# Kernel tuning notes

Measured on AMD Instinct MI355X. Metric: run time of the kernel, lower is better.

The kernel has to match this reference:

```python
import jax, jax.numpy as jnp
import numpy as np

T = 4096
HIDDEN = 2048
N_HEADS = 16
N_KV_HEADS = 4
HEAD_DIM = 128
WINDOW = 1024  # per_layer_sliding_window = WINDOW + 1 -> q attends keys with q_pos - k_pos <= WINDOW
ROPE_THETA = 100000.0
QKV_OUT = (N_HEADS + 2 * N_KV_HEADS) * HEAD_DIM  # 3072


def setup_inputs() -> dict:
    key = jax.random.key(0)
    k1, k2, k3, k4 = jax.random.split(key, 4)
    return {
        "hidden_states": jax.random.normal(k1, (T, HIDDEN), dtype=jnp.float32),
        "positions": jnp.arange(T, dtype=jnp.int32),
        "w_qkv": jax.random.normal(k2, (HIDDEN, QKV_OUT), dtype=jnp.float32) * 0.02,
        "b_qkv": jax.random.normal(k3, (QKV_OUT,), dtype=jnp.float32) * 0.02,
        "w_o": jax.random.normal(k4, (N_HEADS * HEAD_DIM, HIDDEN), dtype=jnp.float32) * 0.02,
    }


def _apply_rope(x, positions):
    # x: [T, n_heads, HEAD_DIM], neox-style rotary over full head dim
    half = HEAD_DIM // 2
    inv_freq = 1.0 / (ROPE_THETA ** (jnp.arange(half, dtype=jnp.float32) / half))
    freqs = positions.astype(jnp.float32)[:, None] * inv_freq[None, :]  # [T, half]
    cos = jnp.cos(freqs)[:, None, :]  # [T, 1, half]
    sin = jnp.sin(freqs)[:, None, :]
    x1, x2 = x[..., :half], x[..., half:]
    return jnp.concatenate([x1 * cos - x2 * sin, x2 * cos + x1 * sin], axis=-1)


def reference(hidden_states, positions, w_qkv, b_qkv, w_o):
    # QKV projection (bias=True)
    qkv = hidden_states @ w_qkv + b_qkv  # [T, QKV_OUT]
    q_size = N_HEADS * HEAD_DIM
    kv_size = N_KV_HEADS * HEAD_DIM
    q = qkv[:, :q_size].reshape(T, N_HEADS, HEAD_DIM)
    k = qkv[:, q_size:q_size + kv_size].reshape(T, N_KV_HEADS, HEAD_DIM)
    v = qkv[:, q_size + kv_size:].reshape(T, N_KV_HEADS, HEAD_DIM)

    # RoPE on q and k
    q = _apply_rope(q, positions)
    k = _apply_rope(k, positions)

    # GQA: expand kv heads to match query heads
    group = N_HEADS // N_KV_HEADS
    k = jnp.repeat(k, group, axis=1)  # [T, N_HEADS, HEAD_DIM]
    v = jnp.repeat(v, group, axis=1)

    scale = HEAD_DIM ** -0.5
    scores = jnp.einsum('qhd,khd->hqk', q, k) * scale  # [H, T, T]

    # causal + sliding-window mask: j <= i and i - j <= WINDOW
    i = jnp.arange(T)[:, None]
    j = jnp.arange(T)[None, :]
    mask = (j <= i) & (i - j <= WINDOW)  # [T, T]
    scores = jnp.where(mask[None, :, :], scores, jnp.finfo(scores.dtype).min)

    probs = jax.nn.softmax(scores, axis=-1)
    attn = jnp.einsum('hqk,khd->qhd', probs, v)  # [T, H, HEAD_DIM]
    attn = attn.reshape(T, N_HEADS * HEAD_DIM)

    # output projection (bias=False)
    return attn @ w_o
```

## Files before the change

kernel.cpp:

```cpp
#include <hip/hip_runtime.h>
#include <cstdint>

#define T_TOK 4096
#define HID 2048
#define NH 16
#define NKV 4
#define HD 128
#define WIN 1024
#define QKVO 3072

typedef float f32x4 __attribute__((ext_vector_type(4)));
typedef __bf16 bf16x8 __attribute__((ext_vector_type(8)));
typedef __bf16 bf16x4 __attribute__((ext_vector_type(4)));
typedef __bf16 bf16x2 __attribute__((ext_vector_type(2)));

__device__ __forceinline__ void gload16(const void* g, void* lds) {
  auto gp = reinterpret_cast<__attribute__((address_space(1))) void*>(
      reinterpret_cast<uintptr_t>(g));
  auto lp = reinterpret_cast<__attribute__((address_space(3))) void*>(
      reinterpret_cast<uintptr_t>(lds));
  __builtin_amdgcn_global_load_lds(gp, lp, 16, 0, 0);
}

__device__ __forceinline__ f32x4 mfma16(bf16x8 a, bf16x8 b, f32x4 c) {
  return __builtin_amdgcn_mfma_f32_16x16x32_bf16(a, b, c, 0, 0, 0);
}

__global__ __launch_bounds__(256) void k_f32_to_bf16(const float* __restrict__ x,
                                                     __bf16* __restrict__ y) {
  const size_t e = (size_t)blockIdx.x * 256 + threadIdx.x;
  const float4* xv = (const float4*)x;
  float4 a = xv[e * 2], b = xv[e * 2 + 1];
  bf16x8 o;
  o[0] = (__bf16)a.x; o[1] = (__bf16)a.y; o[2] = (__bf16)a.z; o[3] = (__bf16)a.w;
  o[4] = (__bf16)b.x; o[5] = (__bf16)b.y; o[6] = (__bf16)b.z; o[7] = (__bf16)b.w;
  *(bf16x8*)(y + e * 8) = o;
}

__global__ __launch_bounds__(256) void k_transpose(const float* __restrict__ W,
                                                   __bf16* __restrict__ Wt,
                                                   int R, int C) {
  __shared__ __bf16 tb[32][33];
  const int nbx = C >> 5;
  const int c0 = (blockIdx.x % nbx) << 5;
  const int r0 = (blockIdx.x / nbx) << 5;
  const int tx = threadIdx.x & 31, ty = threadIdx.x >> 5;
#pragma unroll
  for (int i = 0; i < 32; i += 8)
    tb[ty + i][tx] = (__bf16)W[(size_t)(r0 + ty + i) * C + c0 + tx];
  __syncthreads();
#pragma unroll
  for (int i = 0; i < 32; i += 8)
    Wt[(size_t)(c0 + ty + i) * R + r0 + tx] = tb[tx][ty + i];
}

__global__ void k_rope_tab(const int* __restrict__ pos, float* __restrict__ cosT,
                           float* __restrict__ sinT) {
  const int t = blockIdx.x;
  const int d = threadIdx.x;
  const float inv = exp2f(-(float)d * (16.609640474436812f / 64.0f));
  const float fr = (float)pos[t] * inv;
  cosT[t * 64 + d] = cosf(fr);
  sinT[t * 64 + d] = sinf(fr);
}

template <bool BIAS, typename OutT>
__global__ __launch_bounds__(256, 2) void k_gemm(const __bf16* __restrict__ A,
                                                 const __bf16* __restrict__ Bt,
                                                 const float* __restrict__ bias,
                                                 OutT* __restrict__ C,
                                                 int M, int N, int K) {
  __shared__ __align__(16) __bf16 As[2][128 * 32];
  __shared__ __align__(16) __bf16 Bs[2][128 * 32];
  const int tid = threadIdx.x;
  const int lane = tid & 63;
  const int w = tid >> 6;
  const int wr = w >> 1, wc = w & 1;
  const int c = lane & 15, g = lane >> 4;
  const int gsw = g ^ ((c >> 1) & 3);

  const int nstc = N >> 9;
  const int bid = blockIdx.x;
  const int xcd = bid & 7;
  const int j = bid >> 3;
  const int spx = (int)(gridDim.x >> 7);
  const int s = xcd * spx + (j >> 4);
  const int q = j & 15;
  const int by = (s / nstc) * 4 + (q >> 2);
  const int bx = (s % nstc) * 4 + (q & 3);
  const int m0 = by << 7, n0 = bx << 7;

  const int o0 = w * 2048 + lane * 16;
  const int r0 = o0 >> 6;
  const int g0 = (lane & 3) ^ ((r0 >> 1) & 3);
  const int o1 = o0 + 1024;
  const int r1 = o1 >> 6;
  const int g1 = (lane & 3) ^ ((r1 >> 1) & 3);
  const __bf16* gA0 = A + (size_t)(m0 + r0) * K + g0 * 8;
  const __bf16* gA1 = A + (size_t)(m0 + r1) * K + g1 * 8;
  const __bf16* gB0 = Bt + (size_t)(n0 + r0) * K + g0 * 8;
  const __bf16* gB1 = Bt + (size_t)(n0 + r1) * K + g1 * 8;

  f32x4 acc[4][4] = {};

  {
    char* la = (char*)&As[0][0];
    char* lb = (char*)&Bs[0][0];
    gload16(gA0, la + o0);
    gload16(gA1, la + o1);
    gload16(gB0, lb + o0);
    gload16(gB1, lb + o1);
  }
  __syncthreads();

  int cur = 0;
  for (int kt = 0; kt < K; kt += 32) {
    if (kt + 32 < K) {
      char* la = (char*)&As[0][0] + (cur ^ 1) * 8192;
      char* lb = (char*)&Bs[0][0] + (cur ^ 1) * 8192;
      gload16(gA0 + kt + 32, la + o0);
      gload16(gA1 + kt + 32, la + o1);
      gload16(gB0 + kt + 32, lb + o0);
      gload16(gB1 + kt + 32, lb + o1);
    }
    const __bf16* as = &As[0][0] + cur * 4096;
    const __bf16* bs = &Bs[0][0] + cur * 4096;
    bf16x8 af[4], bfr[4];
#pragma unroll
    for (int mi = 0; mi < 4; mi++)
      af[mi] = *(const bf16x8*)(as + (wr * 64 + mi * 16 + c) * 32 + gsw * 8);
#pragma unroll
    for (int ni = 0; ni < 4; ni++)
      bfr[ni] = *(const bf16x8*)(bs + (wc * 64 + ni * 16 + c) * 32 + gsw * 8);
#pragma unroll
    for (int mi = 0; mi < 4; mi++)
#pragma unroll
      for (int ni = 0; ni < 4; ni++)
        acc[mi][ni] = mfma16(af[mi], bfr[ni], acc[mi][ni]);
    __syncthreads();
    cur ^= 1;
  }

#pragma unroll
  for (int ni = 0; ni < 4; ni++) {
    const int col = n0 + wc * 64 + ni * 16 + c;
    const float bv = BIAS ? bias[col] : 0.0f;
#pragma unroll
    for (int mi = 0; mi < 4; mi++)
#pragma unroll
      for (int r = 0; r < 4; r++) {
        const int row = m0 + wr * 64 + mi * 16 + 4 * g + r;
        C[(size_t)row * N + col] = (OutT)(acc[mi][ni][r] + bv);
      }
  }
}

__global__ __launch_bounds__(256) void k_rope_pack(
    const __bf16* __restrict__ qkv, const float* __restrict__ cosT,
    const float* __restrict__ sinT, __bf16* __restrict__ Qp,
    __bf16* __restrict__ Kp, __bf16* __restrict__ Vt) {
  const int t0 = blockIdx.x * 64;
  const int hh = blockIdx.y;
  const int tid = threadIdx.x;
  const int col0 = hh * HD;
  __shared__ __bf16 lt[64][136];
  if (hh < NH + NKV) {
    const bool isq = hh < NH;
    const float s = isq ? 0.08838834764831845f : 1.0f;
    __bf16* base = isq ? (Qp + (size_t)hh * T_TOK * HD)
                       : (Kp + (size_t)(hh - NH) * T_TOK * HD);
#pragma unroll
    for (int jj = 0; jj < 2; jj++) {
      const int e = jj * 256 + tid;
      const int tl = e >> 3, ch = e & 7;
      const int tt = t0 + tl;
      const bf16x8 x1 = *(const bf16x8*)(qkv + (size_t)tt * QKVO + col0 + ch * 8);
      const bf16x8 x2 = *(const bf16x8*)(qkv + (size_t)tt * QKVO + col0 + 64 + ch * 8);
      const float4 c0 = *(const float4*)(cosT + tt * 64 + ch * 8);
      const float4 c1 = *(const float4*)(cosT + tt * 64 + ch * 8 + 4);
      const float4 s0 = *(const float4*)(sinT + tt * 64 + ch * 8);
      const float4 s1 = *(const float4*)(sinT + tt * 64 + ch * 8 + 4);
      const float cs[8] = {c0.x, c0.y, c0.z, c0.w, c1.x, c1.y, c1.z, c1.w};
      const float sn[8] = {s0.x, s0.y, s0.z, s0.w, s1.x, s1.y, s1.z, s1.w};
      bf16x8 o1, o2;
#pragma unroll
      for (int i = 0; i < 8; i++) {
        const float a = (float)x1[i], b = (float)x2[i];
        o1[i] = (__bf16)((a * cs[i] - b * sn[i]) * s);
        o2[i] = (__bf16)((b * cs[i] + a * sn[i]) * s);
      }
      const int d2s = isq ? ch * 8 : ((ch * 8) ^ ((tt & 7) << 3));
      __bf16* dst = base + (size_t)tt * HD;
      *(bf16x8*)(dst + d2s) = o1;
      *(bf16x8*)(dst + 64 + d2s) = o2;
    }
  } else {
    const int kv = hh - (NH + NKV);
#pragma unroll
    for (int jj = 0; jj < 4; jj++) {
      const int e = jj * 256 + tid;
      const int tl = e >> 4, dc = e & 15;
      *(bf16x8*)&lt[tl][dc * 8] =
          *(const bf16x8*)(qkv + (size_t)(t0 + tl) * QKVO + col0 + dc * 8);
    }
    __syncthreads();
#pragma unroll
    for (int jj = 0; jj < 32; jj++) {
      const int e = jj * 256 + tid;
      const int d = e >> 6, tl = e & 63;
      Vt[((size_t)kv * HD + d) * T_TOK + t0 + (tl ^ ((d & 7) << 3))] = lt[tl][d];
    }
  }
}

__global__ __launch_bounds__(512, 4) void k_attn(const __bf16* __restrict__ Qp,
                                                 const __bf16* __restrict__ Kp,
                                                 const __bf16* __restrict__ Vt,
                                                 __bf16* __restrict__ attnO) {
  __shared__ __align__(16) __bf16 Ks[2][64 * 128];
  __shared__ __align__(16) __bf16 Vs[2][128 * 64];
  __shared__ __align__(16) __bf16 Ps[8][16 * 64];

  const int tid = threadIdx.x;
  const int lane = tid & 63;
  const int w = tid >> 6;
  const int c = lane & 15, g = lane >> 4;
  const int h = blockIdx.y;
  const int kvh = h >> 2;
  const int qb = (int)(gridDim.x - 1) - (int)blockIdx.x;
  const int q0 = qb * 128;
  const int i_row = q0 + w * 16 + c;
  const int swz = (c & 7) << 4;

  bf16x8 qf[4];
  {
    const __bf16* qbase = Qp + ((size_t)h * T_TOK + i_row) * HD;
#pragma unroll
    for (int ds = 0; ds < 4; ds++) qf[ds] = *(const bf16x8*)(qbase + ds * 32 + g * 8);
  }

  f32x4 ot[8] = {};
  float mrun = 0.0f, lrun = 0.0f;

  const int jstart = (q0 >= WIN) ? (q0 - WIN) : 0;
  const int niter = (q0 + 128 - jstart) >> 6;

  const char* Kg = (const char*)Kp + (size_t)kvh * T_TOK * HD * 2;
  const char* Vg = (const char*)Vt + (size_t)kvh * HD * T_TOK * 2;
  const char* kg0 = Kg + (size_t)(jstart + 8 * w + (lane >> 4)) * 256 + (lane & 15) * 16;
  const char* vg0 = Vg + (size_t)(16 * w + (lane >> 3)) * (T_TOK * 2) +
                    (size_t)jstart * 2 + (lane & 7) * 16;

#pragma unroll
  for (int q = 0; q < 2; q++)
    gload16(kg0 + q * 1024, (char*)&Ks[0][0] + w * 2048 + q * 1024);
#pragma unroll
  for (int q = 0; q < 2; q++)
    gload16(vg0 + (size_t)q * 8 * (T_TOK * 2), (char*)&Vs[0][0] + w * 2048 + q * 1024);

  char* pw = (char*)&Ps[w][0];
  int cur = 0;

  for (int it = 0; it < niter; ++it) {
    const int j0 = jstart + it * 64;
    __syncthreads();

    if (it + 1 < niter) {
      const char* kg = kg0 + (size_t)(it + 1) * 16384;
      const char* vg = vg0 + (size_t)(it + 1) * 128;
      char* kd = (char*)&Ks[cur ^ 1][0] + w * 2048;
      char* vd = (char*)&Vs[cur ^ 1][0] + w * 2048;
#pragma unroll
      for (int q = 0; q < 2; q++) gload16(kg + q * 1024, kd + q * 1024);
#pragma unroll
      for (int q = 0; q < 2; q++)
        gload16(vg + (size_t)q * 8 * (T_TOK * 2), vd + q * 1024);
    }

    const char* kb = (const char*)&Ks[cur][0];
    const char* vb = (const char*)&Vs[cur][0];

    f32x4 st[4] = {};
    __builtin_amdgcn_s_setprio(1);
#pragma unroll
    for (int t = 0; t < 4; t++)
#pragma unroll
      for (int ds = 0; ds < 4; ds++) {
        bf16x8 kf = *(const bf16x8*)(kb + (t * 16 + c) * 256 + ((ds * 64 + g * 16) ^ swz));
        st[t] = mfma16(kf, qf[ds], st[t]);
      }
    __builtin_amdgcn_s_setprio(0);

    float p[16];
    float cmax = -1e30f;
    const int jb = i_row - j0 - 4 * g;
#pragma unroll
    for (int t = 0; t < 4; t++)
#pragma unroll
      for (int r = 0; r < 4; r++) {
        float s = st[t][r];
        s = ((unsigned)(jb - 16 * t - r) <= WIN) ? s : -1e30f;
        p[t * 4 + r] = s;
        cmax = fmaxf(cmax, s);
      }
    cmax = fmaxf(cmax, __shfl_xor(cmax, 16));
    cmax = fmaxf(cmax, __shfl_xor(cmax, 32));

    if (!__all(cmax <= mrun + 8.0f)) {
      const float mn = fmaxf(mrun, cmax);
      const float alpha = __expf(mrun - mn);
      lrun *= alpha;
#pragma unroll
      for (int m = 0; m < 8; m++) ot[m] *= alpha;
      mrun = mn;
    }
    float rs = 0.0f;
#pragma unroll
    for (int x = 0; x < 16; x++) {
      const float e_ = __expf(p[x] - mrun);
      p[x] = e_;
      rs += e_;
    }
    rs += __shfl_xor(rs, 16);
    rs += __shfl_xor(rs, 32);
    lrun += rs;

#pragma unroll
    for (int t = 0; t < 4; t++) {
      bf16x4 pk;
      pk[0] = (__bf16)p[t * 4 + 0];
      pk[1] = (__bf16)p[t * 4 + 1];
      pk[2] = (__bf16)p[t * 4 + 2];
      pk[3] = (__bf16)p[t * 4 + 3];
      *(bf16x4*)(pw + c * 128 + ((t * 32 + g * 8) ^ swz)) = pk;
    }
    bf16x8 pf[2];
#pragma unroll
    for (int ks = 0; ks < 2; ks++)
      pf[ks] = *(const bf16x8*)(pw + c * 128 + ((ks * 64 + g * 16) ^ swz));

    __builtin_amdgcn_s_setprio(1);
#pragma unroll
    for (int m = 0; m < 8; m++)
#pragma unroll
      for (int ks = 0; ks < 2; ks++) {
        bf16x8 vf = *(const bf16x8*)(vb + (m * 16 + c) * 128 + ((ks * 64 + g * 16) ^ swz));
        ot[m] = mfma16(vf, pf[ks], ot[m]);
      }
    __builtin_amdgcn_s_setprio(0);

    cur ^= 1;
  }

  const float inv_l = 1.0f / lrun;
  __bf16* orow = attnO + (size_t)i_row * (NH * HD) + h * HD;
#pragma unroll
  for (int m = 0; m < 8; m++) {
    bf16x4 o4;
#pragma unroll
    for (int r = 0; r < 4; r++) o4[r] = (__bf16)(ot[m][r] * inv_l);
    *(bf16x4*)(orow + m * 16 + 4 * g) = o4;
  }
}

extern "C" void kernel_launch(void* const* d_in, const int* in_sizes, int n_in,
                              void* d_out, int out_size, void* d_ws, size_t ws_size,
                              hipStream_t stream) {
  (void)in_sizes; (void)n_in; (void)out_size; (void)ws_size;
  const float* hidden = (const float*)d_in[0];
  const int* positions = (const int*)d_in[1];
  const float* w_qkv = (const float*)d_in[2];
  const float* b_qkv = (const float*)d_in[3];
  const float* w_o = (const float*)d_in[4];
  float* out = (float*)d_out;

  char* ws = (char*)d_ws;
  __bf16* Hb = (__bf16*)ws;    ws += (size_t)T_TOK * HID * 2;
  __bf16* Wqkvt = (__bf16*)ws; ws += (size_t)QKVO * HID * 2;
  __bf16* Wot = (__bf16*)ws;   ws += (size_t)HID * HID * 2;
  float* cosT = (float*)ws;    ws += (size_t)T_TOK * 64 * 4;
  float* sinT = (float*)ws;    ws += (size_t)T_TOK * 64 * 4;
  __bf16* qkv = (__bf16*)ws;   ws += (size_t)T_TOK * QKVO * 2;
  __bf16* Qp = (__bf16*)ws;    ws += (size_t)NH * T_TOK * HD * 2;
  __bf16* Kp = (__bf16*)ws;    ws += (size_t)NKV * T_TOK * HD * 2;
  __bf16* Vt = (__bf16*)ws;    ws += (size_t)NKV * HD * T_TOK * 2;
  __bf16* attnb = (__bf16*)ws; ws += (size_t)T_TOK * NH * HD * 2;

  k_f32_to_bf16<<<T_TOK * HID / (256 * 8), 256, 0, stream>>>(hidden, Hb);
  k_transpose<<<(QKVO / 32) * (HID / 32), 256, 0, stream>>>(w_qkv, Wqkvt, HID, QKVO);
  k_transpose<<<(HID / 32) * (HID / 32), 256, 0, stream>>>(w_o, Wot, HID, HID);
  k_rope_tab<<<T_TOK, 64, 0, stream>>>(positions, cosT, sinT);
  k_gemm<true, __bf16><<<(T_TOK / 128) * (QKVO / 128), 256, 0, stream>>>(
      Hb, Wqkvt, b_qkv, qkv, T_TOK, QKVO, HID);
  k_rope_pack<<<dim3(T_TOK / 64, NH + 2 * NKV), 256, 0, stream>>>(
      qkv, cosT, sinT, Qp, Kp, Vt);
  k_attn<<<dim3(T_TOK / 128, NH), 512, 0, stream>>>(Qp, Kp, Vt, attnb);
  k_gemm<false, float><<<(T_TOK / 128) * (HID / 128), 256, 0, stream>>>(
      attnb, Wot, nullptr, out, T_TOK, HID, HID);
}
```

Baseline: 190.9 us.

## Give each attention wave two query sub-tiles, fold log2e into Q, skip interior masking

The attention kernel drops from 8 waves to 4 waves per block, and each wave now handles 32 query rows as two 16-row sub-tiles. Each K and V fragment read from LDS feeds two MFMAs, which halves LDS fragment traffic per unit of compute. The softmax scale now includes log2(e) so exp2f can replace __expf, and the rescale threshold is adjusted to match. Tiles lying fully inside the causal window skip the per-element mask test. The cost is higher register pressure and fewer waves per block, which may reduce latency hiding.

```diff
diff --git a/kernel.cpp b/kernel.cpp
--- a/kernel.cpp
+++ b/kernel.cpp
@@ -166,7 +166,7 @@
   __shared__ __bf16 lt[64][136];
   if (hh < NH + NKV) {
     const bool isq = hh < NH;
-    const float s = isq ? 0.08838834764831845f : 1.0f;
+    const float s = isq ? (0.08838834764831845f * 1.4426950408889634f) : 1.0f;
     __bf16* base = isq ? (Qp + (size_t)hh * T_TOK * HD)
                        : (Kp + (size_t)(hh - NH) * T_TOK * HD);
 #pragma unroll
@@ -213,13 +213,13 @@
   }
 }
 
-__global__ __launch_bounds__(512, 4) void k_attn(const __bf16* __restrict__ Qp,
+__global__ __launch_bounds__(256, 2) void k_attn(const __bf16* __restrict__ Qp,
                                                  const __bf16* __restrict__ Kp,
                                                  const __bf16* __restrict__ Vt,
                                                  __bf16* __restrict__ attnO) {
   __shared__ __align__(16) __bf16 Ks[2][64 * 128];
   __shared__ __align__(16) __bf16 Vs[2][128 * 64];
-  __shared__ __align__(16) __bf16 Ps[8][16 * 64];
+  __shared__ __align__(16) __bf16 Ps[4][32 * 64];
 
   const int tid = threadIdx.x;
   const int lane = tid & 63;
@@ -229,34 +229,36 @@
   const int kvh = h >> 2;
   const int qb = (int)(gridDim.x - 1) - (int)blockIdx.x;
   const int q0 = qb * 128;
-  const int i_row = q0 + w * 16 + c;
+  const int iw = q0 + 32 * w;
   const int swz = (c & 7) << 4;
 
-  bf16x8 qf[4];
-  {
-    const __bf16* qbase = Qp + ((size_t)h * T_TOK + i_row) * HD;
-#pragma unroll
-    for (int ds = 0; ds < 4; ds++) qf[ds] = *(const bf16x8*)(qbase + ds * 32 + g * 8);
-  }
-
-  f32x4 ot[8] = {};
-  float mrun = 0.0f, lrun = 0.0f;
+  bf16x8 qf[2][4];
+#pragma unroll
+  for (int qh = 0; qh < 2; qh++) {
+    const __bf16* qbase = Qp + ((size_t)h * T_TOK + iw + 16 * qh + c) * HD;
+#pragma unroll
+    for (int ds = 0; ds < 4; ds++)
+      qf[qh][ds] = *(const bf16x8*)(qbase + ds * 32 + g * 8);
+  }
+
+  f32x4 ot[2][8] = {};
+  float mrun[2] = {0.0f, 0.0f}, lrun[2] = {0.0f, 0.0f};
 
   const int jstart = (q0 >= WIN) ? (q0 - WIN) : 0;
   const int niter = (q0 + 128 - jstart) >> 6;
 
   const char* Kg = (const char*)Kp + (size_t)kvh * T_TOK * HD * 2;
   const char* Vg = (const char*)Vt + (size_t)kvh * HD * T_TOK * 2;
-  const char* kg0 = Kg + (size_t)(jstart + 8 * w + (lane >> 4)) * 256 + (lane & 15) * 16;
-  const char* vg0 = Vg + (size_t)(16 * w + (lane >> 3)) * (T_TOK * 2) +
+  const char* kg0 = Kg + (size_t)(jstart + 16 * w + (lane >> 4)) * 256 + (lane & 15) * 16;
+  const char* vg0 = Vg + (size_t)(32 * w + (lane >> 3)) * (T_TOK * 2) +
                     (size_t)jstart * 2 + (lane & 7) * 16;
 
 #pragma unroll
-  for (int q = 0; q < 2; q++)
-    gload16(kg0 + q * 1024, (char*)&Ks[0][0] + w * 2048 + q * 1024);
-#pragma unroll
-  for (int q = 0; q < 2; q++)
-    gload16(vg0 + (size_t)q * 8 * (T_TOK * 2), (char*)&Vs[0][0] + w * 2048 + q * 1024);
+  for (int q = 0; q < 4; q++)
+    gload16(kg0 + q * 1024, (char*)&Ks[0][0] + w * 4096 + q * 1024);
+#pragma unroll
+  for (int q = 0; q < 4; q++)
+    gload16(vg0 + (size_t)q * 8 * (T_TOK * 2), (char*)&Vs[0][0] + w * 4096 + q * 1024);
 
   char* pw = (char*)&Ps[w][0];
   int cur = 0;
@@ -268,76 +270,97 @@
     if (it + 1 < niter) {
       const char* kg = kg0 + (size_t)(it + 1) * 16384;
       const char* vg = vg0 + (size_t)(it + 1) * 128;
-      char* kd = (char*)&Ks[cur ^ 1][0] + w * 2048;
-      char* vd = (char*)&Vs[cur ^ 1][0] + w * 2048;
-#pragma unroll
-      for (int q = 0; q < 2; q++) gload16(kg + q * 1024, kd + q * 1024);
-#pragma unroll
-      for (int q = 0; q < 2; q++)
+      char* kd = (char*)&Ks[cur ^ 1][0] + w * 4096;
+      char* vd = (char*)&Vs[cur ^ 1][0] + w * 4096;
+#pragma unroll
+      for (int q = 0; q < 4; q++) gload16(kg + q * 1024, kd + q * 1024);
+#pragma unroll
+      for (int q = 0; q < 4; q++)
         gload16(vg + (size_t)q * 8 * (T_TOK * 2), vd + q * 1024);
     }
 
     const char* kb = (const char*)&Ks[cur][0];
     const char* vb = (const char*)&Vs[cur][0];
 
-    f32x4 st[4] = {};
+    f32x4 st[2][4] = {};
     __builtin_amdgcn_s_setprio(1);
 #pragma unroll
     for (int t = 0; t < 4; t++)
 #pragma unroll
       for (int ds = 0; ds < 4; ds++) {
         bf16x8 kf = *(const bf16x8*)(kb + (t * 16 + c) * 256 + ((ds * 64 + g * 16) ^ swz));
-        st[t] = mfma16(kf, qf[ds], st[t]);
+        st[0][t] = mfma16(kf, qf[0][ds], st[0][t]);
+        st[1][t] = mfma16(kf, qf[1][ds], st[1][t]);
       }
     __builtin_amdgcn_s_setprio(0);
 
-    float p[16];
-    float cmax = -1e30f;
-    const int jb = i_row - j0 - 4 * g;
-#pragma unroll
-    for (int t = 0; t < 4; t++)
-#pragma unroll
-      for (int r = 0; r < 4; r++) {
-        float s = st[t][r];
-        s = ((unsigned)(jb - 16 * t - r) <= WIN) ? s : -1e30f;
-        p[t * 4 + r] = s;
-        cmax = fmaxf(cmax, s);
-      }
-    cmax = fmaxf(cmax, __shfl_xor(cmax, 16));
-    cmax = fmaxf(cmax, __shfl_xor(cmax, 32));
-
-    if (!__all(cmax <= mrun + 8.0f)) {
-      const float mn = fmaxf(mrun, cmax);
-      const float alpha = __expf(mrun - mn);
-      lrun *= alpha;
-#pragma unroll
-      for (int m = 0; m < 8; m++) ot[m] *= alpha;
-      mrun = mn;
-    }
-    float rs = 0.0f;
-#pragma unroll
-    for (int x = 0; x < 16; x++) {
-      const float e_ = __expf(p[x] - mrun);
-      p[x] = e_;
-      rs += e_;
-    }
-    rs += __shfl_xor(rs, 16);
-    rs += __shfl_xor(rs, 32);
-    lrun += rs;
-
-#pragma unroll
-    for (int t = 0; t < 4; t++) {
-      bf16x4 pk;
-      pk[0] = (__bf16)p[t * 4 + 0];
-      pk[1] = (__bf16)p[t * 4 + 1];
-      pk[2] = (__bf16)p[t * 4 + 2];
-      pk[3] = (__bf16)p[t * 4 + 3];
-      *(bf16x4*)(pw + c * 128 + ((t * 32 + g * 8) ^ swz)) = pk;
-    }
-    bf16x8 pf[2];
-#pragma unroll
-    for (int ks = 0; ks < 2; ks++)
-      pf[ks] = *(const bf16x8*)(pw + c * 128 + ((ks * 64 + g * 16) ^ swz));
+#pragma unroll
+    for (int qh = 0; qh < 2; qh++) {
+      const int rlo = iw + 16 * qh;
+      const int irow = rlo + c;
+      float p[16];
+      float cmax = -1e30f;
+      if ((j0 + 63 <= rlo) && (rlo + 15 - j0 <= WIN)) {
+#pragma unroll
+        for (int t = 0; t < 4; t++)
+#pragma unroll
+          for (int r = 0; r < 4; r++) {
+            const float s = st[qh][t][r];
+            p[t * 4 + r] = s;
+            cmax = fmaxf(cmax, s);
+          }
+      } else {
+        const int jb = irow - j0 - 4 * g;
+#pragma unroll
+        for (int t = 0; t < 4; t++)
+#pragma unroll
+          for (int r = 0; r < 4; r++) {
+            float s = st[qh][t][r];
+            s = ((unsigned)(jb - 16 * t - r) <= WIN) ? s : -1e30f;
+            p[t * 4 + r] = s;
+            cmax = fmaxf(cmax, s);
+          }
+      }
+      cmax = fmaxf(cmax, __shfl_xor(cmax, 16));
+      cmax = fmaxf(cmax, __shfl_xor(cmax, 32));
+
+      if (!__all(cmax <= mrun[qh] + 11.54f)) {
+        const float mn = fmaxf(mrun[qh], cmax);
+        const float alpha = exp2f(mrun[qh] - mn);
+        lrun[qh] *= alpha;
+#pragma unroll
+        for (int m = 0; m < 8; m++) ot[qh][m] *= alpha;
+        mrun[qh] = mn;
+      }
+      float rs = 0.0f;
+#pragma unroll
+      for (int x = 0; x < 16; x++) {
+        const float e_ = exp2f(p[x] - mrun[qh]);
+        p[x] = e_;
+        rs += e_;
+      }
+      rs += __shfl_xor(rs, 16);
+      rs += __shfl_xor(rs, 32);
+      lrun[qh] += rs;
+
+#pragma unroll
+      for (int t = 0; t < 4; t++) {
+        bf16x4 pk;
+        pk[0] = (__bf16)p[t * 4 + 0];
+        pk[1] = (__bf16)p[t * 4 + 1];
+        pk[2] = (__bf16)p[t * 4 + 2];
+        pk[3] = (__bf16)p[t * 4 + 3];
+        *(bf16x4*)(pw + (16 * qh + c) * 128 + ((t * 32 + g * 8) ^ swz)) = pk;
+      }
+    }
+
+    bf16x8 pf[2][2];
+#pragma unroll
+    for (int qh = 0; qh < 2; qh++)
+#pragma unroll
+      for (int ks = 0; ks < 2; ks++)
+        pf[qh][ks] =
+            *(const bf16x8*)(pw + (16 * qh + c) * 128 + ((ks * 64 + g * 16) ^ swz));
 
     __builtin_amdgcn_s_setprio(1);
 #pragma unroll
@@ -345,21 +368,25 @@
 #pragma unroll
       for (int ks = 0; ks < 2; ks++) {
         bf16x8 vf = *(const bf16x8*)(vb + (m * 16 + c) * 128 + ((ks * 64 + g * 16) ^ swz));
-        ot[m] = mfma16(vf, pf[ks], ot[m]);
+        ot[0][m] = mfma16(vf, pf[0][ks], ot[0][m]);
+        ot[1][m] = mfma16(vf, pf[1][ks], ot[1][m]);
       }
     __builtin_amdgcn_s_setprio(0);
 
     cur ^= 1;
   }
 
-  const float inv_l = 1.0f / lrun;
-  __bf16* orow = attnO + (size_t)i_row * (NH * HD) + h * HD;
-#pragma unroll
-  for (int m = 0; m < 8; m++) {
-    bf16x4 o4;
-#pragma unroll
-    for (int r = 0; r < 4; r++) o4[r] = (__bf16)(ot[m][r] * inv_l);
-    *(bf16x4*)(orow + m * 16 + 4 * g) = o4;
+#pragma unroll
+  for (int qh = 0; qh < 2; qh++) {
+    const float inv_l = 1.0f / lrun[qh];
+    __bf16* orow = attnO + (size_t)(iw + 16 * qh + c) * (NH * HD) + h * HD;
+#pragma unroll
+    for (int m = 0; m < 8; m++) {
+      bf16x4 o4;
+#pragma unroll
+      for (int r = 0; r < 4; r++) o4[r] = (__bf16)(ot[qh][m][r] * inv_l);
+      *(bf16x4*)(orow + m * 16 + 4 * g) = o4;
+    }
   }
 }
 
@@ -394,7 +421,7 @@
       Hb, Wqkvt, b_qkv, qkv, T_TOK, QKVO, HID);
   k_rope_pack<<<dim3(T_TOK / 64, NH + 2 * NKV), 256, 0, stream>>>(
       qkv, cosT, sinT, Qp, Kp, Vt);
-  k_attn<<<dim3(T_TOK / 128, NH), 512, 0, stream>>>(Qp, Kp, Vt, attnb);
+  k_attn<<<dim3(T_TOK / 128, NH), 256, 0, stream>>>(Qp, Kp, Vt, attnb);
   k_gemm<false, float><<<(T_TOK / 128) * (HID / 128), 256, 0, stream>>>(
       attnb, Wot, nullptr, out, T_TOK, HID, HID);
 }
```

Measured after the change: 194.8 us. +2.1%, slower.
